# Kernel optimization log

Measured on AMD Instinct MI355X. Metric: run time of the kernel, lower is better.

## Reference

```python
import jax, jax.numpy as jnp
import numpy as np
from jax import lax

N_EMBD = 1024
N_HEAD = 16
HEAD_DIM = N_EMBD // N_HEAD
EPS = 1e-6
B, T = 4, 2048


def setup_inputs() -> dict:
    key = jax.random.key(0)
    ks = jax.random.split(key, 5)
    scale = 1.0 / np.sqrt(N_EMBD)
    return {
        "x": jax.random.normal(ks[0], (B, T, N_EMBD), jnp.float32),
        "W_attn": jax.random.normal(ks[1], (N_EMBD, 3 * N_EMBD), jnp.float32) * scale,
        "b_attn": jax.random.normal(ks[2], (3 * N_EMBD,), jnp.float32) * 0.01,
        "W_proj": jax.random.normal(ks[3], (N_EMBD, N_EMBD), jnp.float32) * scale,
        "b_proj": jax.random.normal(ks[4], (N_EMBD,), jnp.float32) * 0.01,
    }


def _feature_map(x):
    # ELU + 1 for non-negativity
    return jax.nn.elu(x) + 1.0


def reference(x, W_attn, b_attn, W_proj, b_proj):
    Bb, Tt, C = x.shape
    qkv = x @ W_attn + b_attn  # (B,T,3C)
    q, k, v = jnp.split(qkv, 3, axis=-1)

    def to_heads(t):
        # (B,T,C) -> (T,B,H,d): scan axis leading
        return t.reshape(Bb, Tt, N_HEAD, HEAD_DIM).transpose(1, 0, 2, 3)

    q = _feature_map(to_heads(q))
    k = _feature_map(to_heads(k))
    v = to_heads(v)

    # Causal linear attention: O(d^2) running state instead of the torch
    # code's materialized (B,H,T,d,d) cumsum — same math.
    def step(carry, inp):
        kv, ksum = carry  # (B,H,d,d), (B,H,d)
        qt, kt, vt = inp  # each (B,H,d)
        kv = kv + kt[..., :, None] * vt[..., None, :]
        ksum = ksum + kt
        num = jnp.einsum('bhi,bhij->bhj', qt, kv)
        den = jnp.einsum('bhi,bhi->bh', qt, ksum)[..., None] + EPS
        return (kv, ksum), num / den

    init = (
        jnp.zeros((Bb, N_HEAD, HEAD_DIM, HEAD_DIM), x.dtype),
        jnp.zeros((Bb, N_HEAD, HEAD_DIM), x.dtype),
    )
    _, y = lax.scan(step, init, (q, k, v))  # (T,B,H,d)
    y = y.transpose(1, 0, 2, 3).reshape(Bb, Tt, C)
    return y @ W_proj + b_proj  # dropout is identity in eval mode
```

## Files before the change

### kernel.cpp

```cpp
#include <hip/hip_runtime.h>
#include <math.h>

#define BB   4
#define TT   2048
#define CC   1024
#define HH   16
#define DD   64
#define MM   (BB*TT)
#define NQKV (3*CC)
#define LCH  128
#define NCH  (TT/LCH)
#define EPSF 1e-6f

#define PST  136
#define VTST 136

typedef __bf16 bf16x8 __attribute__((ext_vector_type(8)));
typedef float  floatx4 __attribute__((ext_vector_type(4)));

__device__ __forceinline__ unsigned short f2bf(float f) {
  union { float f; unsigned int u; } v; v.f = f;
  unsigned int r = v.u + 0x7fffu + ((v.u >> 16) & 1u);
  return (unsigned short)(r >> 16);
}
__device__ __forceinline__ float bf2f(unsigned short s) {
  union { unsigned int u; float f; } v; v.u = ((unsigned int)s) << 16;
  return v.f;
}
__device__ __forceinline__ float featmap(float v) {
  return v > 0.f ? v + 1.f : __expf(v);
}
__device__ __forceinline__ void gld_lds_b128(const unsigned short* g, unsigned short* l) {
  __builtin_amdgcn_global_load_lds(
      (const __attribute__((address_space(1))) unsigned int*)g,
      (__attribute__((address_space(3))) unsigned int*)l, 16, 0, 0);
}

__device__ __forceinline__ void transpose_cvt_body(const float* __restrict__ W,
                                                   unsigned short* __restrict__ out,
                                                   int R, int Cc, int bx32, int by32, int tid) {
  __shared__ float tile[32][33];
  int bx = bx32 * 32, by = by32 * 32;
  {
    int r = tid >> 3, c4 = tid & 7;
    float4 f = *(const float4*)&W[(size_t)(by + r) * Cc + bx + c4 * 4];
    tile[r][c4 * 4 + 0] = f.x; tile[r][c4 * 4 + 1] = f.y;
    tile[r][c4 * 4 + 2] = f.z; tile[r][c4 * 4 + 3] = f.w;
  }
  __syncthreads();
  {
    int i = tid >> 3, t4 = tid & 7;
    ushort4 o;
    o.x = f2bf(tile[t4 * 4 + 0][i]);
    o.y = f2bf(tile[t4 * 4 + 1][i]);
    o.z = f2bf(tile[t4 * 4 + 2][i]);
    o.w = f2bf(tile[t4 * 4 + 3][i]);
    *(ushort4*)&out[(size_t)(bx + i) * R + by + t4 * 4] = o;
  }
}

__global__ __launch_bounds__(256) void prep_kernel(
    const float* __restrict__ x, unsigned short* __restrict__ xb,
    const float* __restrict__ Wa, unsigned short* __restrict__ WaT,
    const float* __restrict__ Wp, unsigned short* __restrict__ WpT) {
  int blk = blockIdx.x, tid = threadIdx.x;
  if (blk < 8192) {
    int i = (blk * 256 + tid) * 4;
    float4 f = *(const float4*)(x + i);
    ushort4 o;
    o.x = f2bf(f.x); o.y = f2bf(f.y); o.z = f2bf(f.z); o.w = f2bf(f.w);
    *(ushort4*)(xb + i) = o;
  } else if (blk < 8192 + 3072) {
    int t = blk - 8192;
    transpose_cvt_body(Wa, WaT, CC, NQKV, t % 96, t / 96, tid);
  } else {
    int t = blk - 11264;
    transpose_cvt_body(Wp, WpT, CC, CC, t % 32, t / 32, tid);
  }
}

#define BKQ   32
#define ASLT  (256 * BKQ)
#define BSLT  (192 * BKQ)
#define NT_Q  (CC / BKQ)

__global__ __launch_bounds__(512, 2) void gemm_qkv_kernel(
    const unsigned short* __restrict__ A, const unsigned short* __restrict__ Bt,
    const float* __restrict__ bias,
    unsigned short* __restrict__ qh, unsigned short* __restrict__ kh,
    unsigned short* __restrict__ vh) {
  extern __shared__ __align__(16) unsigned short lds[];
  unsigned short* Ar = lds;
  unsigned short* Br = lds + 4 * ASLT;

  const int tid = threadIdx.x;
  const int wave = tid >> 6, lane = tid & 63;
  const int lr = lane & 15, lq = lane >> 4;
  const int lin = blockIdx.y * 16 + blockIdx.x;
  const int lin2 = (lin & 7) * 64 + (lin >> 3);
  const int m0 = (lin2 >> 4) * 256, n0 = (lin2 & 15) * 192;
  const int wm = (wave >> 2) * 128, wn = (wave & 3) * 48;

  const int srow = wave * 16 + (lane >> 2);
  const int cs = (lane & 3) ^ ((lane >> 3) & 3);
  const unsigned short* gA0 = A  + (size_t)(m0 + srow) * CC + cs * 8;
  const unsigned short* gB0 = Bt + (size_t)(n0 + srow) * CC + cs * 8;
  unsigned short* const stA = Ar + wave * 512;
  unsigned short* const stB = Br + wave * 512;
  const bool bhi = (wave < 4);

  const int chunk = lq ^ ((lr >> 1) & 3);
  const int roA = (wm + lr) * BKQ + chunk * 8;
  const int roB = (wn + lr) * BKQ + chunk * 8;

  floatx4 acc[3][8] = {};

#define QSTAGE_A(tt) do {                                      \
    const unsigned short* g_ = gA0 + (tt) * BKQ;               \
    unsigned short* d_ = stA + ((tt) & 3) * ASLT;              \
    gld_lds_b128(g_, d_);                                      \
    gld_lds_b128(g_ + (size_t)128 * CC, d_ + 4096);            \
  } while (0)
#define QSTAGE_B(tt) do {                                      \
    const unsigned short* g_ = gB0 + (tt) * BKQ;               \
    unsigned short* d_ = stB + ((tt) & 3) * BSLT;              \
    gld_lds_b128(g_, d_);                                      \
    if (bhi) gld_lds_b128(g_ + (size_t)128 * CC, d_ + 4096);   \
  } while (0)

  QSTAGE_A(0); QSTAGE_B(0);
  QSTAGE_A(1); QSTAGE_B(1);
  QSTAGE_A(2); QSTAGE_B(2);
  asm volatile("s_waitcnt vmcnt(6)" ::: "memory");
  __builtin_amdgcn_s_barrier();

  #pragma unroll 4
  for (int t = 0; t < NT_Q; ++t) {
    const unsigned short* sA = Ar + (t & 3) * ASLT + roA;
    const unsigned short* sB = Br + (t & 3) * BSLT + roB;
    bf16x8 an[3], bm[8];
    #pragma unroll
    for (int i = 0; i < 3; i++) an[i] = *(const bf16x8*)(sB + i * (16 * BKQ));
    #pragma unroll
    for (int j = 0; j < 8; j++) bm[j] = *(const bf16x8*)(sA + j * (16 * BKQ));
    if (t < NT_Q - 3) { QSTAGE_A(t + 3); QSTAGE_B(t + 3); }
    __builtin_amdgcn_s_barrier();
    asm volatile("s_waitcnt lgkmcnt(0)" ::: "memory");
    __builtin_amdgcn_s_setprio(1);
    #pragma unroll
    for (int i = 0; i < 3; i++)
      #pragma unroll
      for (int j = 0; j < 8; j++)
        acc[i][j] = __builtin_amdgcn_mfma_f32_16x16x32_bf16(an[i], bm[j], acc[i][j], 0, 0, 0);
    __builtin_amdgcn_s_setprio(0);
    if (t < NT_Q - 3)        asm volatile("s_waitcnt vmcnt(6)" ::: "memory");
    else if (t == NT_Q - 3)  asm volatile("s_waitcnt vmcnt(3)" ::: "memory");
    else if (t == NT_Q - 2)  asm volatile("s_waitcnt vmcnt(0)" ::: "memory");
    __builtin_amdgcn_s_barrier();
  }
#undef QSTAGE_A
#undef QSTAGE_B

  unsigned short* dstv[3];
  size_t qoff[3];
  float4 bi[3];
  bool feat[3];
  #pragma unroll
  for (int i = 0; i < 3; i++) {
    const int n = n0 + wn + i * 16 + lq * 4;
    dstv[i] = (n < 1024) ? qh : (n < 2048) ? kh : vh;
    feat[i] = (n < 2048);
    const int h = (n & 1023) >> 6, dd = n & 63;
    qoff[i] = (size_t)h * (TT * DD) + dd;
    bi[i] = *(const float4*)&bias[n];
  }
  #pragma unroll
  for (int j = 0; j < 8; j++) {
    const int m = m0 + wm + j * 16 + lr;
    const int b = m >> 11, tg = m & 2047;
    const size_t pj = (size_t)b * (HH * TT * DD) + (size_t)tg * DD;
    #pragma unroll
    for (int i = 0; i < 3; i++) {
      float v0 = acc[i][j][0] + bi[i].x, v1 = acc[i][j][1] + bi[i].y;
      float v2 = acc[i][j][2] + bi[i].z, v3 = acc[i][j][3] + bi[i].w;
      if (feat[i]) { v0 = featmap(v0); v1 = featmap(v1); v2 = featmap(v2); v3 = featmap(v3); }
      ushort4 o; o.x = f2bf(v0); o.y = f2bf(v1); o.z = f2bf(v2); o.w = f2bf(v3);
      *(ushort4*)&dstv[i][pj + qoff[i]] = o;
    }
  }
}

#define PBK   32
#define PASLT (128 * PBK)
#define PBSLT (256 * PBK)
#define NT_P  (CC / PBK)

__global__ __launch_bounds__(512, 2) void gemm_proj_kernel(
    const unsigned short* __restrict__ A, const unsigned short* __restrict__ Bt,
    const float* __restrict__ bias, float* __restrict__ out) {
  extern __shared__ __align__(16) unsigned short lds[];
  unsigned short* Ar = lds;
  unsigned short* Br = lds + 4 * PASLT;

  const int tid = threadIdx.x;
  const int wave = tid >> 6, lane = tid & 63;
  const int lr = lane & 15, lq = lane >> 4;
  const int lin = blockIdx.y * 4 + blockIdx.x;
  const int lin2 = (lin & 7) * 32 + (lin >> 3);
  const int m0 = (lin2 >> 2) * 128, n0 = (lin2 & 3) * 256;
  const int wm = (wave >> 2) * 64, wn = (wave & 3) * 64;

  const int srow = wave * 16 + (lane >> 2);
  const int cs = (lane & 3) ^ ((lane >> 3) & 3);
  const unsigned short* gA0 = A  + (size_t)(m0 + srow) * CC + cs * 8;
  const unsigned short* gB0 = Bt + (size_t)(n0 + srow) * CC + cs * 8;
  unsigned short* const stA = Ar + wave * 512;
  unsigned short* const stB = Br + wave * 512;

  const int chunk = lq ^ ((lr >> 1) & 3);
  const int roA = (wm + lr) * PBK + chunk * 8;
  const int roB = (wn + lr) * PBK + chunk * 8;

  floatx4 acc[4][4] = {};

#define PSTAGE(tt) do {                                        \
    const unsigned short* ga_ = gA0 + (tt) * PBK;              \
    unsigned short* da_ = stA + ((tt) & 3) * PASLT;            \
    gld_lds_b128(ga_, da_);                                    \
    const unsigned short* gb_ = gB0 + (tt) * PBK;              \
    unsigned short* db_ = stB + ((tt) & 3) * PBSLT;            \
    gld_lds_b128(gb_, db_);                                    \
    gld_lds_b128(gb_ + (size_t)128 * CC, db_ + 4096);          \
  } while (0)

  PSTAGE(0); PSTAGE(1); PSTAGE(2);
  asm volatile("s_waitcnt vmcnt(6)" ::: "memory");
  __builtin_amdgcn_s_barrier();

  #pragma unroll 4
  for (int t = 0; t < NT_P; ++t) {
    const unsigned short* sA = Ar + (t & 3) * PASLT + roA;
    const unsigned short* sB = Br + (t & 3) * PBSLT + roB;
    bf16x8 an[4], bm[4];
    #pragma unroll
    for (int i = 0; i < 4; i++) an[i] = *(const bf16x8*)(sB + i * (16 * PBK));
    #pragma unroll
    for (int j = 0; j < 4; j++) bm[j] = *(const bf16x8*)(sA + j * (16 * PBK));
    if (t < NT_P - 3) PSTAGE(t + 3);
    __builtin_amdgcn_s_barrier();
    asm volatile("s_waitcnt lgkmcnt(0)" ::: "memory");
    __builtin_amdgcn_s_setprio(1);
    #pragma unroll
    for (int i = 0; i < 4; i++)
      #pragma unroll
      for (int j = 0; j < 4; j++)
        acc[i][j] = __builtin_amdgcn_mfma_f32_16x16x32_bf16(an[i], bm[j], acc[i][j], 0, 0, 0);
    __builtin_amdgcn_s_setprio(0);
    if (t < NT_P - 3)        asm volatile("s_waitcnt vmcnt(6)" ::: "memory");
    else if (t == NT_P - 3)  asm volatile("s_waitcnt vmcnt(3)" ::: "memory");
    else if (t == NT_P - 2)  asm volatile("s_waitcnt vmcnt(0)" ::: "memory");
    __builtin_amdgcn_s_barrier();
  }
#undef PSTAGE

  #pragma unroll
  for (int i = 0; i < 4; i++) {
    const int n = n0 + wn + i * 16 + lq * 4;
    const float4 bi = *(const float4*)&bias[n];
    #pragma unroll
    for (int j = 0; j < 4; j++) {
      const int m = m0 + wm + j * 16 + lr;
      float4 o;
      o.x = acc[i][j][0] + bi.x; o.y = acc[i][j][1] + bi.y;
      o.z = acc[i][j][2] + bi.z; o.w = acc[i][j][3] + bi.w;
      *(float4*)&out[(size_t)m * CC + n] = o;
    }
  }
}

__global__ __launch_bounds__(256) void chunk_state_kernel(
    const unsigned short* __restrict__ kh, const unsigned short* __restrict__ vh,
    float* __restrict__ KVx) {
  __shared__ __align__(16) unsigned short Kt[64 * VTST];
  __shared__ __align__(16) unsigned short Vt[80 * VTST];
  int blk = blockIdx.x;
  int bh = blk / NCH, c = blk % NCH;
  int tid = threadIdx.x;
  const unsigned short* kp = kh + ((size_t)bh * TT + c * LCH) * DD;
  const unsigned short* vp = vh + ((size_t)bh * TT + c * LCH) * DD;
  {
    int t = tid & 127, j0 = (tid >> 7) * 8;
    union { uint4 u; unsigned short s[8]; } wk[4], wv[4];
    #pragma unroll
    for (int ii = 0; ii < 4; ii++) {
      wk[ii].u = *(const uint4*)&kp[(size_t)t * DD + j0 + ii * 16];
      wv[ii].u = *(const uint4*)&vp[(size_t)t * DD + j0 + ii * 16];
    }
    #pragma unroll
    for (int ii = 0; ii < 4; ii++) {
      const int j8 = j0 + ii * 16;
      #pragma unroll
      for (int jj = 0; jj < 8; jj++) {
        Kt[(j8 + jj) * VTST + t] = wk[ii].s[jj];
        Vt[(j8 + jj) * VTST + t] = wv[ii].s[jj];
      }
    }
  }
  for (int e = tid; e < 16 * 128; e += 256) {
    int rr = e >> 7, n = e & 127;
    Vt[(64 + rr) * VTST + n] = (rr == 0) ? (unsigned short)0x3F80 : (unsigned short)0;
  }
  __syncthreads();
  int wave = tid >> 6, lane = tid & 63;
  int lr = lane & 15, lq = lane >> 4;
  int i0 = wave * 16;
  floatx4 acc[5] = {};
  #pragma unroll
  for (int kk = 0; kk < 4; kk++) {
    bf16x8 a = *(const bf16x8*)&Kt[(i0 + lr) * VTST + kk * 32 + lq * 8];
    #pragma unroll
    for (int jt = 0; jt < 5; jt++) {
      bf16x8 b = *(const bf16x8*)&Vt[(jt * 16 + lr) * VTST + kk * 32 + lq * 8];
      acc[jt] = __builtin_amdgcn_mfma_f32_16x16x32_bf16(a, b, acc[jt], 0, 0, 0);
    }
  }
  float* o = KVx + (size_t)blk * 5120;
  #pragma unroll
  for (int jt = 0; jt < 5; jt++)
    *(float4*)&o[(jt * 16 + lr) * 64 + i0 + lq * 4] = *(float4*)&acc[jt];
}

__global__ __launch_bounds__(256) void prefix_state_kernel(const float* __restrict__ KVx,
                                                           unsigned short* __restrict__ SPb) {
  int bh = blockIdx.x / 5, jb = blockIdx.x % 5;
  int e = jb * 1024 + threadIdx.x * 4;
  size_t base0 = ((size_t)bh * NCH) * 5120 + e;
  float4 v[NCH];
  #pragma unroll
  for (int c = 0; c < NCH; c++)
    v[c] = *(const float4*)&KVx[base0 + (size_t)c * 5120];
  float r0 = 0.f, r1 = 0.f, r2 = 0.f, r3 = 0.f;
  #pragma unroll
  for (int c = 0; c < NCH; c++) {
    ushort4 o;
    o.x = f2bf(r0); o.y = f2bf(r1); o.z = f2bf(r2); o.w = f2bf(r3);
    *(ushort4*)&SPb[base0 + (size_t)c * 5120] = o;
    r0 += v[c].x; r1 += v[c].y; r2 += v[c].z; r3 += v[c].w;
  }
}

__global__ __launch_bounds__(256) void chunk_attn_kernel(
    const unsigned short* __restrict__ qh, const unsigned short* __restrict__ kh,
    const unsigned short* __restrict__ vh, const unsigned short* __restrict__ SPb,
    unsigned short* __restrict__ yb) {
  __shared__ __align__(16) unsigned short lds[17408 + 80 * VTST];
  unsigned short* Qs = lds;
  unsigned short* Ks = lds + 8192;
  unsigned short* P  = lds;
  unsigned short* Vt = lds + 17408;

  int blk = blockIdx.x;
  int bh = blk / NCH, c = blk % NCH;
  int b = bh / HH, h = bh % HH;
  int tid = threadIdx.x;
  const unsigned short* qp = qh + ((size_t)bh * TT + c * LCH) * DD;
  const unsigned short* kp = kh + ((size_t)bh * TT + c * LCH) * DD;
  const unsigned short* vp = vh + ((size_t)bh * TT + c * LCH) * DD;

  int wave = tid >> 6, lane = tid & 63;
  int lr = lane & 15, lq = lane >> 4;
  int mbase = wave * 32;

  const int vt = tid & 127, vj0 = (tid >> 7) * 8;
  uint4 wv[4];
  #pragma unroll
  for (int ii = 0; ii < 4; ii++)
    wv[ii] = *(const uint4*)&vp[(size_t)vt * DD + vj0 + ii * 16];
  asm volatile("" ::: "memory");

  {
    const int grow8 = lane >> 3;
    const int gc = (lane & 7) ^ grow8;
    const unsigned short* gq = qp + (size_t)(wave * 32 + grow8) * DD + gc * 8;
    const unsigned short* gk = kp + (size_t)(wave * 32 + grow8) * DD + gc * 8;
    unsigned short* dq = Qs + wave * 32 * DD;
    unsigned short* dk = Ks + wave * 32 * DD;
    #pragma unroll
    for (int g = 0; g < 4; g++) {
      gld_lds_b128(gq + (size_t)g * 8 * DD, dq + g * 512);
      gld_lds_b128(gk + (size_t)g * 8 * DD, dk + g * 512);
    }
  }

  #pragma unroll
  for (int ii = 0; ii < 4; ii++) {
    union { uint4 u; unsigned short s[8]; } w; w.u = wv[ii];
    const int j8 = vj0 + ii * 16;
    #pragma unroll
    for (int jj = 0; jj < 8; jj++) Vt[(j8 + jj) * VTST + vt] = w.s[jj];
  }
  for (int e = tid; e < 16 * 128; e += 256) {
    int rr = e >> 7, n = e & 127;
    Vt[(64 + rr) * VTST + n] = (rr == 0) ? (unsigned short)0x3F80 : (unsigned short)0;
  }
  asm volatile("s_waitcnt vmcnt(0)" ::: "memory");
  __syncthreads();

  bf16x8 aq[2][2];
  #pragma unroll
  for (int i = 0; i < 2; i++)
    #pragma unroll
    for (int kk = 0; kk < 2; kk++)
      aq[i][kk] = *(const bf16x8*)&Qs[(mbase + i * 16 + lr) * DD +
                                      ((((kk << 2) + lq) ^ (lr & 7)) << 3)];

  floatx4 accT[5][2] = {};
  const unsigned short* spb = SPb + (size_t)blk * (80 * 64);
  #pragma unroll
  for (int jt = 0; jt < 5; jt++)
    #pragma unroll
    for (int kk = 0; kk < 2; kk++) {
      bf16x8 asp = *(const bf16x8*)&spb[(jt * 16 + lr) * 64 + kk * 32 + lq * 8];
      accT[jt][0] = __builtin_amdgcn_mfma_f32_16x16x32_bf16(asp, aq[0][kk], accT[jt][0], 0, 0, 0);
      accT[jt][1] = __builtin_amdgcn_mfma_f32_16x16x32_bf16(asp, aq[1][kk], accT[jt][1], 0, 0, 0);
    }
  floatx4 sacc[2][8] = {};
  #pragma unroll
  for (int nt = 0; nt < 8; nt++)
    #pragma unroll
    for (int kk = 0; kk < 2; kk++) {
      bf16x8 bk = *(const bf16x8*)&Ks[(nt * 16 + lr) * DD +
                                      ((((kk << 2) + lq) ^ (lr & 7)) << 3)];
      sacc[0][nt] = __builtin_amdgcn_mfma_f32_16x16x32_bf16(aq[0][kk], bk, sacc[0][nt], 0, 0, 0);
      sacc[1][nt] = __builtin_amdgcn_mfma_f32_16x16x32_bf16(aq[1][kk], bk, sacc[1][nt], 0, 0, 0);
    }
  __syncthreads();

  #pragma unroll
  for (int i = 0; i < 2; i++)
    #pragma unroll
    for (int nt = 0; nt < 8; nt++) {
      int col = nt * 16 + lr;
      #pragma unroll
      for (int r = 0; r < 4; r++) {
        int m = mbase + i * 16 + lq * 4 + r;
        float v = (col <= m) ? sacc[i][nt][r] : 0.f;
        P[m * PST + col] = f2bf(v);
      }
    }
  __syncthreads();

  #pragma unroll
  for (int kk4 = 0; kk4 < 4; kk4++) {
    bf16x8 bp0 = *(const bf16x8*)&P[(mbase + lr) * PST + kk4 * 32 + lq * 8];
    bf16x8 bp1 = *(const bf16x8*)&P[(mbase + 16 + lr) * PST + kk4 * 32 + lq * 8];
    #pragma unroll
    for (int jt = 0; jt < 5; jt++) {
      bf16x8 av = *(const bf16x8*)&Vt[(jt * 16 + lr) * VTST + kk4 * 32 + lq * 8];
      accT[jt][0] = __builtin_amdgcn_mfma_f32_16x16x32_bf16(av, bp0, accT[jt][0], 0, 0, 0);
      accT[jt][1] = __builtin_amdgcn_mfma_f32_16x16x32_bf16(av, bp1, accT[jt][1], 0, 0, 0);
    }
  }

  #pragma unroll
  for (int it = 0; it < 2; it++) {
    float den = __shfl(accT[4][it][0], lr, 64);
    float inv = 1.f / (den + EPSF);
    int tg = c * LCH + mbase + it * 16 + lr;
    size_t base = ((size_t)b * TT + tg) * CC + h * DD;
    #pragma unroll
    for (int jt = 0; jt < 4; jt++) {
      ushort4 o;
      o.x = f2bf(accT[jt][it][0] * inv);
      o.y = f2bf(accT[jt][it][1] * inv);
      o.z = f2bf(accT[jt][it][2] * inv);
      o.w = f2bf(accT[jt][it][3] * inv);
      *(ushort4*)&yb[base + jt * 16 + lq * 4] = o;
    }
  }
}

extern "C" void kernel_launch(void* const* d_in, const int* in_sizes, int n_in,
                              void* d_out, int out_size, void* d_ws, size_t ws_size,
                              hipStream_t stream) {
  const float* x      = (const float*)d_in[0];
  const float* W_attn = (const float*)d_in[1];
  const float* b_attn = (const float*)d_in[2];
  const float* W_proj = (const float*)d_in[3];
  const float* b_proj = (const float*)d_in[4];
  float* out = (float*)d_out;

  char* ws = (char*)d_ws;
  size_t off = 0;
  auto alloc = [&](size_t bytes) -> char* {
    char* p = ws + off;
    off += (bytes + 255) & ~(size_t)255;
    return p;
  };
  unsigned short* xb  = (unsigned short*)alloc((size_t)MM * CC * 2);
  unsigned short* WaT = (unsigned short*)alloc((size_t)NQKV * CC * 2);
  unsigned short* WpT = (unsigned short*)alloc((size_t)CC * CC * 2);
  unsigned short* qh  = (unsigned short*)alloc((size_t)MM * CC * 2);
  unsigned short* kh  = (unsigned short*)alloc((size_t)MM * CC * 2);
  unsigned short* vh  = (unsigned short*)alloc((size_t)MM * CC * 2);
  float* KVx = (float*)alloc((size_t)BB * HH * NCH * 80 * 64 * 4);
  unsigned short* SPb = (unsigned short*)alloc((size_t)BB * HH * NCH * 80 * 64 * 2);
  unsigned short* yb = xb;

  static bool s_attr_done = false;
  if (!s_attr_done) {
    (void)hipFuncSetAttribute((const void*)gemm_qkv_kernel,
                              hipFuncAttributeMaxDynamicSharedMemorySize, 114688);
    (void)hipFuncSetAttribute((const void*)gemm_proj_kernel,
                              hipFuncAttributeMaxDynamicSharedMemorySize, 98304);
    s_attr_done = true;
  }

  prep_kernel<<<12288, 256, 0, stream>>>(x, xb, W_attn, WaT, W_proj, WpT);
  gemm_qkv_kernel<<<dim3(NQKV / 192, MM / 256), 512, 114688, stream>>>(xb, WaT, b_attn, qh, kh, vh);
  chunk_state_kernel<<<BB * HH * NCH, 256, 0, stream>>>(kh, vh, KVx);
  prefix_state_kernel<<<BB * HH * 5, 256, 0, stream>>>(KVx, SPb);
  chunk_attn_kernel<<<BB * HH * NCH, 256, 0, stream>>>(qh, kh, vh, SPb, yb);
  gemm_proj_kernel<<<dim3(CC / 256, MM / 128), 512, 98304, stream>>>(yb, WpT, b_proj, out);
}
```

Baseline: 217.7 us.

## Fuse chunk state, prefix scan and chunk attention into one sequential kernel

Replaces the three-kernel chunked linear attention (per-chunk KV state, prefix scan over chunks, per-chunk attention) with a single kernel where each block owns one (batch, head) and loops over chunks, keeping the running KV state in registers and staging it in LDS as bf16. This removes two launches and the global round trip of per-chunk states and prefix sums. In exchange the grid shrinks to one block per head, serialising the chunk loop and leaving most compute units idle, with no overlap between chunk loads and compute.

```diff
diff --git a/kernel.cpp b/kernel.cpp
--- a/kernel.cpp
+++ b/kernel.cpp
@@ -14,6 +14,7 @@
 
 #define PST  136
 #define VTST 136
+#define SST  72
 
 typedef __bf16 bf16x8 __attribute__((ext_vector_type(8)));
 typedef float  floatx4 __attribute__((ext_vector_type(4)));
@@ -278,205 +279,170 @@
   }
 }
 
-__global__ __launch_bounds__(256) void chunk_state_kernel(
-    const unsigned short* __restrict__ kh, const unsigned short* __restrict__ vh,
-    float* __restrict__ KVx) {
-  __shared__ __align__(16) unsigned short Kt[64 * VTST];
-  __shared__ __align__(16) unsigned short Vt[80 * VTST];
-  int blk = blockIdx.x;
-  int bh = blk / NCH, c = blk % NCH;
-  int tid = threadIdx.x;
-  const unsigned short* kp = kh + ((size_t)bh * TT + c * LCH) * DD;
-  const unsigned short* vp = vh + ((size_t)bh * TT + c * LCH) * DD;
-  {
-    int t = tid & 127, j0 = (tid >> 7) * 8;
-    union { uint4 u; unsigned short s[8]; } wk[4], wv[4];
-    #pragma unroll
-    for (int ii = 0; ii < 4; ii++) {
-      wk[ii].u = *(const uint4*)&kp[(size_t)t * DD + j0 + ii * 16];
-      wv[ii].u = *(const uint4*)&vp[(size_t)t * DD + j0 + ii * 16];
-    }
-    #pragma unroll
-    for (int ii = 0; ii < 4; ii++) {
-      const int j8 = j0 + ii * 16;
-      #pragma unroll
-      for (int jj = 0; jj < 8; jj++) {
-        Kt[(j8 + jj) * VTST + t] = wk[ii].s[jj];
-        Vt[(j8 + jj) * VTST + t] = wv[ii].s[jj];
-      }
-    }
-  }
+__global__ __launch_bounds__(256) void fused_attn_kernel(
+    const unsigned short* __restrict__ qh, const unsigned short* __restrict__ kh,
+    const unsigned short* __restrict__ vh, unsigned short* __restrict__ yb) {
+  extern __shared__ __align__(16) unsigned short flds[];
+  unsigned short* Qs = flds;
+  unsigned short* Ks = flds + 8192;
+  unsigned short* Kt = flds + 16384;
+  unsigned short* Vt = flds + 25088;
+  unsigned short* Sb = flds + 35968;
+  unsigned short* P  = flds + 41728;
+
+  const int bh = blockIdx.x;
+  const int b = bh / HH, h = bh % HH;
+  const int tid = threadIdx.x;
+  const int wave = tid >> 6, lane = tid & 63;
+  const int lr = lane & 15, lq = lane >> 4;
+  const int mbase = wave * 32;
+  const int i0 = wave * 16;
+
+  const unsigned short* qp0 = qh + (size_t)bh * TT * DD;
+  const unsigned short* kp0 = kh + (size_t)bh * TT * DD;
+  const unsigned short* vp0 = vh + (size_t)bh * TT * DD;
+
   for (int e = tid; e < 16 * 128; e += 256) {
     int rr = e >> 7, n = e & 127;
     Vt[(64 + rr) * VTST + n] = (rr == 0) ? (unsigned short)0x3F80 : (unsigned short)0;
   }
-  __syncthreads();
-  int wave = tid >> 6, lane = tid & 63;
-  int lr = lane & 15, lq = lane >> 4;
-  int i0 = wave * 16;
-  floatx4 acc[5] = {};
-  #pragma unroll
-  for (int kk = 0; kk < 4; kk++) {
-    bf16x8 a = *(const bf16x8*)&Kt[(i0 + lr) * VTST + kk * 32 + lq * 8];
+
+  floatx4 run[5] = {};
+
+  const int vt = tid & 127, vj0 = (tid >> 7) * 8;
+  const int grow8 = lane >> 3;
+  const int gc = (lane & 7) ^ grow8;
+
+  for (int c = 0; c < NCH; ++c) {
+    const unsigned short* qp = qp0 + (size_t)c * LCH * DD;
+    const unsigned short* kp = kp0 + (size_t)c * LCH * DD;
+    const unsigned short* vp = vp0 + (size_t)c * LCH * DD;
+
     #pragma unroll
     for (int jt = 0; jt < 5; jt++) {
-      bf16x8 b = *(const bf16x8*)&Vt[(jt * 16 + lr) * VTST + kk * 32 + lq * 8];
-      acc[jt] = __builtin_amdgcn_mfma_f32_16x16x32_bf16(a, b, acc[jt], 0, 0, 0);
-    }
-  }
-  float* o = KVx + (size_t)blk * 5120;
-  #pragma unroll
-  for (int jt = 0; jt < 5; jt++)
-    *(float4*)&o[(jt * 16 + lr) * 64 + i0 + lq * 4] = *(float4*)&acc[jt];
-}
-
-__global__ __launch_bounds__(256) void prefix_state_kernel(const float* __restrict__ KVx,
-                                                           unsigned short* __restrict__ SPb) {
-  int bh = blockIdx.x / 5, jb = blockIdx.x % 5;
-  int e = jb * 1024 + threadIdx.x * 4;
-  size_t base0 = ((size_t)bh * NCH) * 5120 + e;
-  float4 v[NCH];
-  #pragma unroll
-  for (int c = 0; c < NCH; c++)
-    v[c] = *(const float4*)&KVx[base0 + (size_t)c * 5120];
-  float r0 = 0.f, r1 = 0.f, r2 = 0.f, r3 = 0.f;
-  #pragma unroll
-  for (int c = 0; c < NCH; c++) {
-    ushort4 o;
-    o.x = f2bf(r0); o.y = f2bf(r1); o.z = f2bf(r2); o.w = f2bf(r3);
-    *(ushort4*)&SPb[base0 + (size_t)c * 5120] = o;
-    r0 += v[c].x; r1 += v[c].y; r2 += v[c].z; r3 += v[c].w;
-  }
-}
-
-__global__ __launch_bounds__(256) void chunk_attn_kernel(
-    const unsigned short* __restrict__ qh, const unsigned short* __restrict__ kh,
-    const unsigned short* __restrict__ vh, const unsigned short* __restrict__ SPb,
-    unsigned short* __restrict__ yb) {
-  __shared__ __align__(16) unsigned short lds[17408 + 80 * VTST];
-  unsigned short* Qs = lds;
-  unsigned short* Ks = lds + 8192;
-  unsigned short* P  = lds;
-  unsigned short* Vt = lds + 17408;
-
-  int blk = blockIdx.x;
-  int bh = blk / NCH, c = blk % NCH;
-  int b = bh / HH, h = bh % HH;
-  int tid = threadIdx.x;
-  const unsigned short* qp = qh + ((size_t)bh * TT + c * LCH) * DD;
-  const unsigned short* kp = kh + ((size_t)bh * TT + c * LCH) * DD;
-  const unsigned short* vp = vh + ((size_t)bh * TT + c * LCH) * DD;
-
-  int wave = tid >> 6, lane = tid & 63;
-  int lr = lane & 15, lq = lane >> 4;
-  int mbase = wave * 32;
-
-  const int vt = tid & 127, vj0 = (tid >> 7) * 8;
-  uint4 wv[4];
-  #pragma unroll
-  for (int ii = 0; ii < 4; ii++)
-    wv[ii] = *(const uint4*)&vp[(size_t)vt * DD + vj0 + ii * 16];
-  asm volatile("" ::: "memory");
-
-  {
-    const int grow8 = lane >> 3;
-    const int gc = (lane & 7) ^ grow8;
-    const unsigned short* gq = qp + (size_t)(wave * 32 + grow8) * DD + gc * 8;
-    const unsigned short* gk = kp + (size_t)(wave * 32 + grow8) * DD + gc * 8;
-    unsigned short* dq = Qs + wave * 32 * DD;
-    unsigned short* dk = Ks + wave * 32 * DD;
-    #pragma unroll
-    for (int g = 0; g < 4; g++) {
-      gld_lds_b128(gq + (size_t)g * 8 * DD, dq + g * 512);
-      gld_lds_b128(gk + (size_t)g * 8 * DD, dk + g * 512);
-    }
-  }
-
-  #pragma unroll
-  for (int ii = 0; ii < 4; ii++) {
-    union { uint4 u; unsigned short s[8]; } w; w.u = wv[ii];
-    const int j8 = vj0 + ii * 16;
-    #pragma unroll
-    for (int jj = 0; jj < 8; jj++) Vt[(j8 + jj) * VTST + vt] = w.s[jj];
-  }
-  for (int e = tid; e < 16 * 128; e += 256) {
-    int rr = e >> 7, n = e & 127;
-    Vt[(64 + rr) * VTST + n] = (rr == 0) ? (unsigned short)0x3F80 : (unsigned short)0;
-  }
-  asm volatile("s_waitcnt vmcnt(0)" ::: "memory");
-  __syncthreads();
-
-  bf16x8 aq[2][2];
-  #pragma unroll
-  for (int i = 0; i < 2; i++)
-    #pragma unroll
-    for (int kk = 0; kk < 2; kk++)
-      aq[i][kk] = *(const bf16x8*)&Qs[(mbase + i * 16 + lr) * DD +
-                                      ((((kk << 2) + lq) ^ (lr & 7)) << 3)];
-
-  floatx4 accT[5][2] = {};
-  const unsigned short* spb = SPb + (size_t)blk * (80 * 64);
-  #pragma unroll
-  for (int jt = 0; jt < 5; jt++)
-    #pragma unroll
-    for (int kk = 0; kk < 2; kk++) {
-      bf16x8 asp = *(const bf16x8*)&spb[(jt * 16 + lr) * 64 + kk * 32 + lq * 8];
-      accT[jt][0] = __builtin_amdgcn_mfma_f32_16x16x32_bf16(asp, aq[0][kk], accT[jt][0], 0, 0, 0);
-      accT[jt][1] = __builtin_amdgcn_mfma_f32_16x16x32_bf16(asp, aq[1][kk], accT[jt][1], 0, 0, 0);
-    }
-  floatx4 sacc[2][8] = {};
-  #pragma unroll
-  for (int nt = 0; nt < 8; nt++)
-    #pragma unroll
-    for (int kk = 0; kk < 2; kk++) {
-      bf16x8 bk = *(const bf16x8*)&Ks[(nt * 16 + lr) * DD +
-                                      ((((kk << 2) + lq) ^ (lr & 7)) << 3)];
-      sacc[0][nt] = __builtin_amdgcn_mfma_f32_16x16x32_bf16(aq[0][kk], bk, sacc[0][nt], 0, 0, 0);
-      sacc[1][nt] = __builtin_amdgcn_mfma_f32_16x16x32_bf16(aq[1][kk], bk, sacc[1][nt], 0, 0, 0);
-    }
-  __syncthreads();
-
-  #pragma unroll
-  for (int i = 0; i < 2; i++)
-    #pragma unroll
-    for (int nt = 0; nt < 8; nt++) {
-      int col = nt * 16 + lr;
-      #pragma unroll
-      for (int r = 0; r < 4; r++) {
-        int m = mbase + i * 16 + lq * 4 + r;
-        float v = (col <= m) ? sacc[i][nt][r] : 0.f;
-        P[m * PST + col] = f2bf(v);
-      }
-    }
-  __syncthreads();
-
-  #pragma unroll
-  for (int kk4 = 0; kk4 < 4; kk4++) {
-    bf16x8 bp0 = *(const bf16x8*)&P[(mbase + lr) * PST + kk4 * 32 + lq * 8];
-    bf16x8 bp1 = *(const bf16x8*)&P[(mbase + 16 + lr) * PST + kk4 * 32 + lq * 8];
-    #pragma unroll
-    for (int jt = 0; jt < 5; jt++) {
-      bf16x8 av = *(const bf16x8*)&Vt[(jt * 16 + lr) * VTST + kk4 * 32 + lq * 8];
-      accT[jt][0] = __builtin_amdgcn_mfma_f32_16x16x32_bf16(av, bp0, accT[jt][0], 0, 0, 0);
-      accT[jt][1] = __builtin_amdgcn_mfma_f32_16x16x32_bf16(av, bp1, accT[jt][1], 0, 0, 0);
-    }
-  }
-
-  #pragma unroll
-  for (int it = 0; it < 2; it++) {
-    float den = __shfl(accT[4][it][0], lr, 64);
-    float inv = 1.f / (den + EPSF);
-    int tg = c * LCH + mbase + it * 16 + lr;
-    size_t base = ((size_t)b * TT + tg) * CC + h * DD;
-    #pragma unroll
-    for (int jt = 0; jt < 4; jt++) {
       ushort4 o;
-      o.x = f2bf(accT[jt][it][0] * inv);
-      o.y = f2bf(accT[jt][it][1] * inv);
-      o.z = f2bf(accT[jt][it][2] * inv);
-      o.w = f2bf(accT[jt][it][3] * inv);
-      *(ushort4*)&yb[base + jt * 16 + lq * 4] = o;
-    }
+      o.x = f2bf(run[jt][0]); o.y = f2bf(run[jt][1]);
+      o.z = f2bf(run[jt][2]); o.w = f2bf(run[jt][3]);
+      *(ushort4*)&Sb[(jt * 16 + lr) * SST + i0 + lq * 4] = o;
+    }
+
+    uint4 wv[4], wk[4];
+    #pragma unroll
+    for (int ii = 0; ii < 4; ii++) {
+      wv[ii] = *(const uint4*)&vp[(size_t)vt * DD + vj0 + ii * 16];
+      wk[ii] = *(const uint4*)&kp[(size_t)vt * DD + vj0 + ii * 16];
+    }
+    asm volatile("" ::: "memory");
+
+    {
+      const unsigned short* gq = qp + (size_t)(mbase + grow8) * DD + gc * 8;
+      const unsigned short* gk = kp + (size_t)(mbase + grow8) * DD + gc * 8;
+      unsigned short* dq = Qs + mbase * DD;
+      unsigned short* dk = Ks + mbase * DD;
+      #pragma unroll
+      for (int g = 0; g < 4; g++) {
+        gld_lds_b128(gq + (size_t)g * 8 * DD, dq + g * 512);
+        gld_lds_b128(gk + (size_t)g * 8 * DD, dk + g * 512);
+      }
+    }
+    #pragma unroll
+    for (int ii = 0; ii < 4; ii++) {
+      union { uint4 u; unsigned short s[8]; } w1, w2; w1.u = wv[ii]; w2.u = wk[ii];
+      const int j8 = vj0 + ii * 16;
+      #pragma unroll
+      for (int jj = 0; jj < 8; jj++) {
+        Vt[(j8 + jj) * VTST + vt] = w1.s[jj];
+        Kt[(j8 + jj) * VTST + vt] = w2.s[jj];
+      }
+    }
+    asm volatile("s_waitcnt vmcnt(0)" ::: "memory");
+    __syncthreads();
+
+    bf16x8 aq[2][2];
+    #pragma unroll
+    for (int i = 0; i < 2; i++)
+      #pragma unroll
+      for (int kk = 0; kk < 2; kk++)
+        aq[i][kk] = *(const bf16x8*)&Qs[(mbase + i * 16 + lr) * DD +
+                                        ((((kk << 2) + lq) ^ (lr & 7)) << 3)];
+
+    floatx4 accT[5][2] = {};
+    #pragma unroll
+    for (int jt = 0; jt < 5; jt++)
+      #pragma unroll
+      for (int kk = 0; kk < 2; kk++) {
+        bf16x8 asp = *(const bf16x8*)&Sb[(jt * 16 + lr) * SST + kk * 32 + lq * 8];
+        accT[jt][0] = __builtin_amdgcn_mfma_f32_16x16x32_bf16(asp, aq[0][kk], accT[jt][0], 0, 0, 0);
+        accT[jt][1] = __builtin_amdgcn_mfma_f32_16x16x32_bf16(asp, aq[1][kk], accT[jt][1], 0, 0, 0);
+      }
+    floatx4 sacc[2][8] = {};
+    #pragma unroll
+    for (int nt = 0; nt < 8; nt++)
+      #pragma unroll
+      for (int kk = 0; kk < 2; kk++) {
+        bf16x8 bk = *(const bf16x8*)&Ks[(nt * 16 + lr) * DD +
+                                        ((((kk << 2) + lq) ^ (lr & 7)) << 3)];
+        sacc[0][nt] = __builtin_amdgcn_mfma_f32_16x16x32_bf16(aq[0][kk], bk, sacc[0][nt], 0, 0, 0);
+        sacc[1][nt] = __builtin_amdgcn_mfma_f32_16x16x32_bf16(aq[1][kk], bk, sacc[1][nt], 0, 0, 0);
+      }
+
+    #pragma unroll
+    for (int i = 0; i < 2; i++)
+      #pragma unroll
+      for (int nt = 0; nt < 8; nt++) {
+        int col = nt * 16 + lr;
+        #pragma unroll
+        for (int r = 0; r < 4; r++) {
+          int m = mbase + i * 16 + lq * 4 + r;
+          float v = (col <= m) ? sacc[i][nt][r] : 0.f;
+          P[m * PST + col] = f2bf(v);
+        }
+      }
+    __syncthreads();
+
+    #pragma unroll
+    for (int kk4 = 0; kk4 < 4; kk4++) {
+      bf16x8 bp0 = *(const bf16x8*)&P[(mbase + lr) * PST + kk4 * 32 + lq * 8];
+      bf16x8 bp1 = *(const bf16x8*)&P[(mbase + 16 + lr) * PST + kk4 * 32 + lq * 8];
+      #pragma unroll
+      for (int jt = 0; jt < 5; jt++) {
+        bf16x8 av = *(const bf16x8*)&Vt[(jt * 16 + lr) * VTST + kk4 * 32 + lq * 8];
+        accT[jt][0] = __builtin_amdgcn_mfma_f32_16x16x32_bf16(av, bp0, accT[jt][0], 0, 0, 0);
+        accT[jt][1] = __builtin_amdgcn_mfma_f32_16x16x32_bf16(av, bp1, accT[jt][1], 0, 0, 0);
+      }
+    }
+
+    #pragma unroll
+    for (int it = 0; it < 2; it++) {
+      float den = __shfl(accT[4][it][0], lr, 64);
+      float inv = 1.f / (den + EPSF);
+      int tg = c * LCH + mbase + it * 16 + lr;
+      size_t base = ((size_t)b * TT + tg) * CC + h * DD;
+      #pragma unroll
+      for (int jt = 0; jt < 4; jt++) {
+        ushort4 o;
+        o.x = f2bf(accT[jt][it][0] * inv);
+        o.y = f2bf(accT[jt][it][1] * inv);
+        o.z = f2bf(accT[jt][it][2] * inv);
+        o.w = f2bf(accT[jt][it][3] * inv);
+        *(ushort4*)&yb[base + jt * 16 + lq * 4] = o;
+      }
+    }
+
+    floatx4 ca[5] = {};
+    #pragma unroll
+    for (int kk = 0; kk < 4; kk++) {
+      bf16x8 a = *(const bf16x8*)&Kt[(i0 + lr) * VTST + kk * 32 + lq * 8];
+      #pragma unroll
+      for (int jt = 0; jt < 5; jt++) {
+        bf16x8 bv = *(const bf16x8*)&Vt[(jt * 16 + lr) * VTST + kk * 32 + lq * 8];
+        ca[jt] = __builtin_amdgcn_mfma_f32_16x16x32_bf16(a, bv, ca[jt], 0, 0, 0);
+      }
+    }
+    #pragma unroll
+    for (int jt = 0; jt < 5; jt++) run[jt] += ca[jt];
+
+    __syncthreads();
   }
 }
 
@@ -503,8 +469,6 @@
   unsigned short* qh  = (unsigned short*)alloc((size_t)MM * CC * 2);
   unsigned short* kh  = (unsigned short*)alloc((size_t)MM * CC * 2);
   unsigned short* vh  = (unsigned short*)alloc((size_t)MM * CC * 2);
-  float* KVx = (float*)alloc((size_t)BB * HH * NCH * 80 * 64 * 4);
-  unsigned short* SPb = (unsigned short*)alloc((size_t)BB * HH * NCH * 80 * 64 * 2);
   unsigned short* yb = xb;
 
   static bool s_attr_done = false;
@@ -513,13 +477,13 @@
                               hipFuncAttributeMaxDynamicSharedMemorySize, 114688);
     (void)hipFuncSetAttribute((const void*)gemm_proj_kernel,
                               hipFuncAttributeMaxDynamicSharedMemorySize, 98304);
+    (void)hipFuncSetAttribute((const void*)fused_attn_kernel,
+                              hipFuncAttributeMaxDynamicSharedMemorySize, 118272);
     s_attr_done = true;
   }
 
   prep_kernel<<<12288, 256, 0, stream>>>(x, xb, W_attn, WaT, W_proj, WpT);
   gemm_qkv_kernel<<<dim3(NQKV / 192, MM / 256), 512, 114688, stream>>>(xb, WaT, b_attn, qh, kh, vh);
-  chunk_state_kernel<<<BB * HH * NCH, 256, 0, stream>>>(kh, vh, KVx);
-  prefix_state_kernel<<<BB * HH * 5, 256, 0, stream>>>(KVx, SPb);
-  chunk_attn_kernel<<<BB * HH * NCH, 256, 0, stream>>>(qh, kh, vh, SPb, yb);
+  fused_attn_kernel<<<BB * HH, 256, 118272, stream>>>(qh, kh, vh, yb);
   gemm_proj_kernel<<<dim3(CC / 256, MM / 128), 512, 98304, stream>>>(yb, WpT, b_proj, out);
 }
```

Result: slower. 284.7 us (+30.8%).
